# Kernel tuning notes

Measured on AMD Instinct MI355X. Metric: run time of the kernel, lower is better.

Reference implementation:

```python
import jax, jax.numpy as jnp
import numpy as np

N = 50000
E = 800000
D_IN = 128
D_HID = 512
D_OUT = 128
BN_EPS = 1e-5


def setup_inputs() -> dict:
    key = jax.random.key(0)
    ks = jax.random.split(key, 12)
    inp = {}
    inp["v"] = jax.random.normal(ks[0], (N, D_IN), dtype=jnp.float32)
    inp["src"] = jax.random.randint(ks[1], (E,), 0, N, dtype=jnp.int32)
    inp["dst"] = jax.random.randint(ks[2], (E,), 0, N, dtype=jnp.int32)
    inp["edge_weight"] = jax.random.uniform(ks[3], (E,), dtype=jnp.float32)
    # learned parameters
    inp["epsilon"] = jnp.zeros((1, 1), dtype=jnp.float32)  # nn.Parameter([[0.0]])
    s1 = 1.0 / np.sqrt(D_IN)
    s2 = 1.0 / np.sqrt(D_HID)
    inp["W1"] = jax.random.uniform(ks[4], (D_IN, D_HID), minval=-s1, maxval=s1, dtype=jnp.float32)
    inp["b1"] = jax.random.uniform(ks[5], (D_HID,), minval=-s1, maxval=s1, dtype=jnp.float32)
    inp["gamma1"] = jnp.ones((D_HID,), dtype=jnp.float32)
    inp["beta1"] = jnp.zeros((D_HID,), dtype=jnp.float32)
    inp["W2"] = jax.random.uniform(ks[6], (D_HID, D_OUT), minval=-s2, maxval=s2, dtype=jnp.float32)
    inp["b2"] = jax.random.uniform(ks[7], (D_OUT,), minval=-s2, maxval=s2, dtype=jnp.float32)
    inp["gamma2"] = jnp.ones((D_OUT,), dtype=jnp.float32)
    inp["beta2"] = jnp.zeros((D_OUT,), dtype=jnp.float32)
    return inp


def _batchnorm(x, gamma, beta):
    # training-mode BN: batch mean / biased variance over the node axis
    mean = jnp.mean(x, axis=0)
    var = jnp.mean(jnp.square(x - mean), axis=0)
    return gamma * (x - mean) * jax.lax.rsqrt(var + BN_EPS) + beta


def reference(v, src, dst, edge_weight, epsilon, W1, b1, gamma1, beta1, W2, b2, gamma2, beta2):
    n = v.shape[0]
    # sparse.mm(a, v): out[dst] += w * v[src]
    msgs = v[src] * edge_weight[:, None]               # [E, D_IN]
    v_agg = jax.ops.segment_sum(msgs, dst, num_segments=n)  # [N, D_IN]
    v_agg = v_agg + epsilon * v                        # epsilon residual
    h = jax.nn.relu(_batchnorm(v_agg @ W1 + b1, gamma1, beta1))
    out = jax.nn.relu(_batchnorm(h @ W2 + b2, gamma2, beta2))
    return out
```

## Files before the change

### kernel.cpp

```cpp
#include <hip/hip_runtime.h>

#define N_NODES 50000
#define E_EDGES 800000
#define D_INF   128
#define D_HIDF  512
#define D_OUTF  128
#define SCAN_NB ((N_NODES + 255) / 256)
#define M1BLKS  ((N_NODES + 255) / 256)
#define FBLKS   ((N_NODES + 63) / 64)
#define EQ8     (E_EDGES / 8)

#define HIST_NB  ((EQ8 + 255) / 256)
#define CAST_NB  3125
#define PREPW_NB 256
#define PREP_ALL_NB (HIST_NB + CAST_NB + 2 * PREPW_NB)

typedef unsigned short u16;
typedef __attribute__((ext_vector_type(8))) short short8;
typedef __attribute__((ext_vector_type(4))) float floatx4;
typedef const __attribute__((address_space(1))) void gas_t;
typedef __attribute__((address_space(3))) void las_t;

__device__ __forceinline__ u16 f2bf(float f) {
    union { float f; unsigned u; } v; v.f = f;
    unsigned r = (v.u + 0x7fffu + ((v.u >> 16) & 1u)) >> 16;
    return (u16)r;
}
__device__ __forceinline__ float bf2f(u16 b) {
    union { unsigned u; float f; } v; v.u = ((unsigned)b) << 16; return v.f;
}

__global__ __launch_bounds__(256) void prep_all_kernel(
        const float* __restrict__ v, const float* __restrict__ W1,
        const float* __restrict__ W2, const int* __restrict__ dst,
        u16* __restrict__ vbf, u16* __restrict__ W1t, u16* __restrict__ W2t,
        int* __restrict__ counts, int* __restrict__ pos) {
    int b = blockIdx.x;
    int tid = threadIdx.x;
    if (b < HIST_NB) {
        int t = b * 256 + tid;
        if (t >= EQ8) return;
        int d[8], p[8];
#pragma unroll
        for (int k = 0; k < 8; ++k) d[k] = dst[t + k * EQ8];
#pragma unroll
        for (int k = 0; k < 8; ++k) p[k] = atomicAdd(&counts[d[k]], 1);
#pragma unroll
        for (int k = 0; k < 8; ++k) pos[t + k * EQ8] = p[k];
    } else if (b < HIST_NB + CAST_NB) {
        int i = (b - HIST_NB) * 256 + tid;
        const float4 a = ((const float4*)v)[i * 2];
        const float4 c = ((const float4*)v)[i * 2 + 1];
        u16 o[8];
        o[0] = f2bf(a.x); o[1] = f2bf(a.y); o[2] = f2bf(a.z); o[3] = f2bf(a.w);
        o[4] = f2bf(c.x); o[5] = f2bf(c.y); o[6] = f2bf(c.z); o[7] = f2bf(c.w);
        ((float4*)vbf)[i] = *(const float4*)o;
    } else if (b < HIST_NB + CAST_NB + PREPW_NB) {
        int idx = (b - HIST_NB - CAST_NB) * 256 + tid;
        int k1 = idx >> 9, n1 = idx & 511;
        W1t[n1 * 128 + k1] = f2bf(W1[idx]);
    } else {
        int idx = (b - HIST_NB - CAST_NB - PREPW_NB) * 256 + tid;
        int k2 = idx >> 7, n2 = idx & 127;
        W2t[n2 * 512 + k2] = f2bf(W2[idx]);
    }
}

__global__ __launch_bounds__(256) void reduce_kernel(const int* __restrict__ counts,
                                                     int* __restrict__ block_sums) {
    __shared__ int lsum[4];
    int tid = threadIdx.x;
    int gid = blockIdx.x * 256 + tid;
    int s = (gid < N_NODES) ? counts[gid] : 0;
#pragma unroll
    for (int off = 32; off; off >>= 1) s += __shfl_down(s, off);
    if ((tid & 63) == 0) lsum[tid >> 6] = s;
    __syncthreads();
    if (tid == 0) block_sums[blockIdx.x] = lsum[0] + lsum[1] + lsum[2] + lsum[3];
}

__global__ __launch_bounds__(256) void scan_final(const int* __restrict__ counts,
                                                  const int* __restrict__ block_sums,
                                                  int* __restrict__ row_start) {
    __shared__ int sh[256];
    __shared__ int bs[256];
    int tid = threadIdx.x;
    int gid = blockIdx.x * 256 + tid;
    sh[tid] = (gid < N_NODES) ? counts[gid] : 0;
    bs[tid] = (tid < SCAN_NB) ? block_sums[tid] : 0;
    __syncthreads();
    for (int off = 1; off < 256; off <<= 1) {
        int t1 = (tid >= off) ? sh[tid - off] : 0;
        int t2 = (tid >= off) ? bs[tid - off] : 0;
        __syncthreads();
        sh[tid] += t1;
        bs[tid] += t2;
        __syncthreads();
    }
    int boff = (blockIdx.x == 0) ? 0 : bs[blockIdx.x - 1];
    int excl = (tid == 0) ? 0 : sh[tid - 1];
    if (gid < N_NODES) row_start[gid] = boff + excl;
    if (gid == 0) row_start[N_NODES] = E_EDGES;
}

__global__ void fill_kernel(const int* __restrict__ src, const int* __restrict__ dst,
                            const float* __restrict__ w, const int* __restrict__ pos,
                            const int* __restrict__ row_start,
                            int2* __restrict__ csr_ew) {
    int e = blockIdx.x * blockDim.x + threadIdx.x;
    if (e >= E_EDGES) return;
    int d = dst[e];
    int idx = row_start[d] + pos[e];
    int2 rec;
    rec.x = src[e];
    rec.y = __float_as_int(w[e]);
    csr_ew[idx] = rec;
}

__global__ __launch_bounds__(256) void gather_kernel(const u16* __restrict__ vbf,
                                                     const int* __restrict__ row_start,
                                                     const int2* __restrict__ csr_ew,
                                                     const float* __restrict__ eps_p,
                                                     u16* __restrict__ vagg) {
    int node = blockIdx.x * 16 + (threadIdx.x >> 4);
    if (node >= N_NODES) return;
    int c8 = (threadIdx.x & 15) << 3;
    int beg = row_start[node];
    int end = row_start[node + 1];
    float a[8] = {};
    int j = beg;
    for (; j + 1 < end; j += 2) {
        int2 e0 = csr_ew[j];
        int2 e1 = csr_ew[j + 1];
        float w0 = __int_as_float(e0.y);
        float w1 = __int_as_float(e1.y);
        float4 r0 = *(const float4*)(vbf + (size_t)e0.x * D_INF + c8);
        float4 r1 = *(const float4*)(vbf + (size_t)e1.x * D_INF + c8);
        const u16* p0 = (const u16*)&r0;
        const u16* p1 = (const u16*)&r1;
#pragma unroll
        for (int t = 0; t < 8; ++t) a[t] += w0 * bf2f(p0[t]);
#pragma unroll
        for (int t = 0; t < 8; ++t) a[t] += w1 * bf2f(p1[t]);
    }
    if (j < end) {
        int2 e0 = csr_ew[j];
        float w0 = __int_as_float(e0.y);
        float4 r0 = *(const float4*)(vbf + (size_t)e0.x * D_INF + c8);
        const u16* p0 = (const u16*)&r0;
#pragma unroll
        for (int t = 0; t < 8; ++t) a[t] += w0 * bf2f(p0[t]);
    }
    float e = eps_p[0];
    float4 rn = *(const float4*)(vbf + (size_t)node * D_INF + c8);
    const u16* pn = (const u16*)&rn;
    u16 o[8];
#pragma unroll
    for (int t = 0; t < 8; ++t) o[t] = f2bf(a[t] + e * bf2f(pn[t]));
    *(float4*)(vagg + (size_t)node * D_INF + c8) = *(const float4*)o;
}

__global__ __launch_bounds__(512) void stats_gemm1(
        const u16* __restrict__ A, const u16* __restrict__ Bt,
        const float* __restrict__ bias,
        float* __restrict__ psum, float* __restrict__ psq, int M) {
    __shared__ __align__(16) char smem[24576];
    u16* As = (u16*)smem;
    u16* Bs = (u16*)(smem + 16384);
    const int bm = blockIdx.y * 256;
    const int bn = blockIdx.x * 128;
    const int tid = threadIdx.x;
    const int wave = tid >> 6, lane = tid & 63;
    const int wr = wave >> 1, wc = wave & 1;
    const int wm = wr * 64, wn = wc * 64;
    const int lm = lane & 15, quad = lane >> 4;
    floatx4 acc[4][4] = {};
    for (int ks = 0; ks < 4; ++ks) {
        const int k0 = ks << 5;
        {
            const int sub = lane >> 2, s = lane & 3;
#pragma unroll
            for (int t = 0; t < 3; ++t) {
                int ch = wave * 3 + t;
                if (ch < 16) {
                    int row = ch * 16 + sub;
                    int grow = bm + row; if (grow > M - 1) grow = M - 1;
                    int ss = s ^ (row & 3);
                    __builtin_amdgcn_global_load_lds(
                        (gas_t*)(A + (size_t)grow * 128 + k0 + ss * 8),
                        (las_t*)(As + row * 32 + s * 8), 16, 0, 0);
                } else {
                    int row = (ch - 16) * 16 + sub;
                    int ss = s ^ (row & 3);
                    __builtin_amdgcn_global_load_lds(
                        (gas_t*)(Bt + (size_t)(bn + row) * 128 + k0 + ss * 8),
                        (las_t*)(Bs + row * 32 + s * 8), 16, 0, 0);
                }
            }
        }
        __syncthreads();
        short8 af[4], bfr[4];
#pragma unroll
        for (int i = 0; i < 4; ++i) {
            int row = wm + i * 16 + lm;
            af[i] = *(const short8*)&As[row * 32 + ((quad ^ (row & 3)) * 8)];
        }
#pragma unroll
        for (int j = 0; j < 4; ++j) {
            int row = wn + j * 16 + lm;
            bfr[j] = *(const short8*)&Bs[row * 32 + ((quad ^ (row & 3)) * 8)];
        }
#pragma unroll
        for (int i = 0; i < 4; ++i)
#pragma unroll
            for (int j = 0; j < 4; ++j)
                acc[i][j] = __builtin_amdgcn_mfma_f32_16x16x32_bf16(af[i], bfr[j], acc[i][j], 0, 0, 0);
        __syncthreads();
    }
    float* redS = (float*)smem;
    float* redQ = redS + 128;
    if (tid < 128) { redS[tid] = 0.f; redQ[tid] = 0.f; }
    __syncthreads();
#pragma unroll
    for (int j = 0; j < 4; ++j) {
        int cl = wn + j * 16 + lm;
        float bj = bias[bn + cl];
        float s = 0.f, q = 0.f;
#pragma unroll
        for (int i = 0; i < 4; ++i) {
            int row0 = bm + wm + i * 16 + quad * 4;
#pragma unroll
            for (int r = 0; r < 4; ++r)
                if (row0 + r < M) { float x = acc[i][j][r] + bj; s += x; q += x * x; }
        }
        s += __shfl_xor(s, 16); q += __shfl_xor(q, 16);
        s += __shfl_xor(s, 32); q += __shfl_xor(q, 32);
        if (quad == 0) { atomicAdd(&redS[cl], s); atomicAdd(&redQ[cl], q); }
    }
    __syncthreads();
    if (tid < 128) {
        psum[(size_t)blockIdx.y * 512 + bn + tid] = redS[tid];
        psq [(size_t)blockIdx.y * 512 + bn + tid] = redQ[tid];
    }
}

__global__ __launch_bounds__(512, 4) void fused_mlp(
        const u16* __restrict__ vagg, const u16* __restrict__ W1t,
        const u16* __restrict__ W2t,
        const float* __restrict__ b1, const float* __restrict__ scale1,
        const float* __restrict__ shift1, const float* __restrict__ b2,
        u16* __restrict__ x2, float* __restrict__ psum, float* __restrict__ psq,
        int M) {
    __shared__ __align__(16) char smem[49152];
    u16* As  = (u16*)smem;
    u16* W1s = (u16*)(smem + 16384);
    u16* W2s = (u16*)smem;
    u16* hs  = (u16*)(smem + 16384);
    const int bm = blockIdx.x * 64;
    const int tid = threadIdx.x;
    const int wave = tid >> 6, lane = tid & 63;
    const int wr = wave >> 2, wc = wave & 3;
    const int wm = wr * 32;
    const int wn1 = wc * 128;
    const int wn2 = wc * 32;
    const int lm = lane & 15, quad = lane >> 4;

    floatx4 acc1[2][8] = {};
    floatx4 acc2[2][2] = {};

    auto stage_w1 = [&](int win) {
#pragma unroll
        for (int u = 0; u < 4; ++u) {
            int c = tid + u * 512;
            int col = c >> 2, s = c & 3;
            __builtin_amdgcn_global_load_lds(
                (gas_t*)(W1t + (size_t)col * 128 + win * 32 + ((s ^ (col & 3)) * 8)),
                (las_t*)(W1s + col * 32 + s * 8), 16, 0, 0);
        }
    };
    auto stage_w2 = [&](int p, int w) {
#pragma unroll
        for (int u = 0; u < 2; ++u) {
            int c = tid + u * 512;
            int n = c >> 3, s = c & 7;
            __builtin_amdgcn_global_load_lds(
                (gas_t*)(W2t + (size_t)n * 512 + w * 128 + p * 64 + ((s ^ (n & 7)) * 8)),
                (las_t*)(W2s + n * 64 + s * 8), 16, 0, 0);
        }
    };
    auto compute1 = [&](int win) {
        short8 a[2], b[8];
#pragma unroll
        for (int i = 0; i < 2; ++i) {
            int row = wm + i * 16 + lm;
            a[i] = *(const short8*)&As[row * 128 + (((win * 4 + quad) ^ (row & 7)) * 8)];
        }
#pragma unroll
        for (int j = 0; j < 8; ++j) {
            int col = wn1 + j * 16 + lm;
            b[j] = *(const short8*)&W1s[col * 32 + ((quad ^ (col & 3)) * 8)];
        }
#pragma unroll
        for (int i = 0; i < 2; ++i)
#pragma unroll
            for (int j = 0; j < 8; ++j)
                acc1[i][j] = __builtin_amdgcn_mfma_f32_16x16x32_bf16(a[i], b[j], acc1[i][j], 0, 0, 0);
    };
    auto compute2 = [&](int w, int ks) {
        short8 a[2], b[2];
#pragma unroll
        for (int i = 0; i < 2; ++i) {
            int row = wm + i * 16 + lm;
            a[i] = *(const short8*)&hs[row * 256 + (((w * 8 + ks * 4 + quad) ^ (row & 7)) * 8)];
        }
#pragma unroll
        for (int j = 0; j < 2; ++j) {
            int n = wn2 + j * 16 + lm;
            b[j] = *(const short8*)&W2s[n * 64 + (((ks * 4 + quad) ^ (n & 7)) * 8)];
        }
#pragma unroll
        for (int i = 0; i < 2; ++i)
#pragma unroll
            for (int j = 0; j < 2; ++j)
                acc2[i][j] = __builtin_amdgcn_mfma_f32_16x16x32_bf16(a[i], b[j], acc2[i][j], 0, 0, 0);
    };
    auto store_h = [&](int p) {
        float hsc[4], hsh[4];
#pragma unroll
        for (int j = 0; j < 4; ++j) {
            int col = wn1 + (p * 4 + j) * 16 + lm;
            float sc = scale1[col];
            hsc[j] = sc;
            hsh[j] = shift1[col] + sc * b1[col];
        }
#pragma unroll
        for (int i = 0; i < 2; ++i)
#pragma unroll
            for (int j = 0; j < 4; ++j)
#pragma unroll
                for (int r = 0; r < 4; ++r) {
                    int row = wm + i * 16 + quad * 4 + r;
                    int kp = wc * 64 + j * 16 + lm;
                    float hv = fmaxf(0.f, acc1[i][p * 4 + j][r] * hsc[j] + hsh[j]);
                    hs[row * 256 + (((kp >> 3) ^ (row & 7)) * 8) + (kp & 7)] = f2bf(hv);
                }
    };

#pragma unroll
    for (int u = 0; u < 2; ++u) {
        int c = tid + u * 512;
        int row = c >> 4, s = c & 15;
        int grow = bm + row; if (grow > M - 1) grow = M - 1;
        __builtin_amdgcn_global_load_lds(
            (gas_t*)(vagg + (size_t)grow * 128 + ((s ^ (row & 7)) * 8)),
            (las_t*)(As + row * 128 + s * 8), 16, 0, 0);
    }
    stage_w1(0);
    __syncthreads();
    compute1(0);
    __syncthreads();
    stage_w1(1);
    __syncthreads();
    compute1(1);
    __syncthreads();
    stage_w1(2);
    __syncthreads();
    compute1(2);
    __syncthreads();
    stage_w1(3);
    __syncthreads();
    compute1(3);
    __syncthreads();

#pragma unroll
    for (int p = 0; p < 2; ++p) {
        stage_w2(p, 0);
        store_h(p);
        __syncthreads();
#pragma unroll
        for (int w = 0; w < 4; ++w) {
            compute2(w, 0); compute2(w, 1);
            __syncthreads();
            if (w < 3) { stage_w2(p, w + 1); __syncthreads(); }
        }
    }

    float* redS = (float*)smem;
    float* redQ = redS + 128;
    if (tid < 128) { redS[tid] = 0.f; redQ[tid] = 0.f; }
    __syncthreads();
    float bj2[2];
#pragma unroll
    for (int j = 0; j < 2; ++j) {
        int cl = wn2 + j * 16 + lm;
        bj2[j] = b2[cl];
        float s = 0.f, q = 0.f;
#pragma unroll
        for (int i = 0; i < 2; ++i) {
            int row0 = bm + wm + i * 16 + quad * 4;
#pragma unroll
            for (int r = 0; r < 4; ++r)
                if (row0 + r < M) { float x = acc2[i][j][r] + bj2[j]; s += x; q += x * x; }
        }
        s += __shfl_xor(s, 16); q += __shfl_xor(q, 16);
        s += __shfl_xor(s, 32); q += __shfl_xor(q, 32);
        if (quad == 0) { atomicAdd(&redS[cl], s); atomicAdd(&redQ[cl], q); }
    }
    __syncthreads();
    if (tid < 128) {
        psum[(size_t)blockIdx.x * 128 + tid] = redS[tid];
        psq [(size_t)blockIdx.x * 128 + tid] = redQ[tid];
    }
    __syncthreads();

    float* obuf = (float*)smem;
#pragma unroll
    for (int i = 0; i < 2; ++i)
#pragma unroll
        for (int j = 0; j < 2; ++j)
#pragma unroll
            for (int r = 0; r < 4; ++r) {
                int row = wm + i * 16 + quad * 4 + r;
                int col = wn2 + j * 16 + lm;
                obuf[row * 132 + col] = acc2[i][j][r] + bj2[j];
            }
    __syncthreads();
    {
        int row = tid >> 3, seg = (tid & 7) * 16;
        int grow = bm + row;
        if (grow < M) {
            u16 ob[16];
#pragma unroll
            for (int t = 0; t < 4; ++t) {
                float4 f = *(float4*)&obuf[row * 132 + seg + t * 4];
                ob[t * 4 + 0] = f2bf(f.x);
                ob[t * 4 + 1] = f2bf(f.y);
                ob[t * 4 + 2] = f2bf(f.z);
                ob[t * 4 + 3] = f2bf(f.w);
            }
            u16* dp = x2 + (size_t)grow * 128 + seg;
            *(float4*)dp       = *(float4*)ob;
            *(float4*)(dp + 8) = *(float4*)(ob + 8);
        }
    }
}

__global__ __launch_bounds__(1024) void bn_finalize_kernel(
        const float* __restrict__ psum, const float* __restrict__ psq,
        const float* __restrict__ gamma, const float* __restrict__ beta,
        float* __restrict__ scale, float* __restrict__ shift,
        int nblocks, int Ncols, float inv_n) {
    __shared__ float shS[16][64];
    __shared__ float shQ[16][64];
    const int tx = threadIdx.x;
    const int ty = threadIdx.y;
    const int c = blockIdx.x * 64 + tx;
    float s = 0.f, q = 0.f;
    for (int b = ty; b < nblocks; b += 16) {
        s += psum[(size_t)b * Ncols + c];
        q += psq [(size_t)b * Ncols + c];
    }
    shS[ty][tx] = s;
    shQ[ty][tx] = q;
    __syncthreads();
    if (ty == 0) {
        float S = 0.f, Q = 0.f;
#pragma unroll
        for (int r = 0; r < 16; ++r) { S += shS[r][tx]; Q += shQ[r][tx]; }
        float m = S * inv_n;
        float var = Q * inv_n - m * m;
        float rs = rsqrtf(var + 1e-5f);
        float sc = gamma[c] * rs;
        scale[c] = sc;
        shift[c] = beta[c] - sc * m;
    }
}

__global__ void bn2_apply_kernel(const u16* __restrict__ X, float* __restrict__ Y,
                                 const float* __restrict__ scale,
                                 const float* __restrict__ shift, int n8) {
    int i = blockIdx.x * blockDim.x + threadIdx.x;
    if (i >= n8) return;
    int c = (i & 15) << 3;
    float4 raw = ((const float4*)X)[i];
    const u16* xb = (const u16*)&raw;
    float4 sc0 = *(const float4*)(scale + c);
    float4 sc1 = *(const float4*)(scale + c + 4);
    float4 sh0 = *(const float4*)(shift + c);
    float4 sh1 = *(const float4*)(shift + c + 4);
    float4 y0, y1;
    y0.x = fmaxf(0.f, bf2f(xb[0]) * sc0.x + sh0.x);
    y0.y = fmaxf(0.f, bf2f(xb[1]) * sc0.y + sh0.y);
    y0.z = fmaxf(0.f, bf2f(xb[2]) * sc0.z + sh0.z);
    y0.w = fmaxf(0.f, bf2f(xb[3]) * sc0.w + sh0.w);
    y1.x = fmaxf(0.f, bf2f(xb[4]) * sc1.x + sh1.x);
    y1.y = fmaxf(0.f, bf2f(xb[5]) * sc1.y + sh1.y);
    y1.z = fmaxf(0.f, bf2f(xb[6]) * sc1.z + sh1.z);
    y1.w = fmaxf(0.f, bf2f(xb[7]) * sc1.w + sh1.w);
    ((float4*)Y)[i * 2]     = y0;
    ((float4*)Y)[i * 2 + 1] = y1;
}

extern "C" void kernel_launch(void* const* d_in, const int* in_sizes, int n_in,
                              void* d_out, int out_size, void* d_ws, size_t ws_size,
                              hipStream_t stream) {
    const float* v    = (const float*)d_in[0];
    const int* src    = (const int*)d_in[1];
    const int* dst    = (const int*)d_in[2];
    const float* ew   = (const float*)d_in[3];
    const float* eps  = (const float*)d_in[4];
    const float* W1   = (const float*)d_in[5];
    const float* b1   = (const float*)d_in[6];
    const float* g1   = (const float*)d_in[7];
    const float* be1  = (const float*)d_in[8];
    const float* W2   = (const float*)d_in[9];
    const float* b2   = (const float*)d_in[10];
    const float* g2   = (const float*)d_in[11];
    const float* be2  = (const float*)d_in[12];
    float* out = (float*)d_out;

    char* base = (char*)d_ws;
    u16* vbf  = (u16*)(base + 51200000ull);
    u16* vagg = (u16*)(base + 64000000ull);
    u16* x2   = (u16*)(base + 76800000ull);
    u16* W1t  = (u16*)(base + 89600000ull);
    u16* W2t  = (u16*)(base + 89731072ull);
    float* psum   = (float*)(base + 89862144ull);
    float* psq    = (float*)(base + 90663168ull);
    float* scale1 = (float*)(base + 91464192ull);
    float* shift1 = scale1 + 512;
    float* scale2 = shift1 + 512;
    float* shift2 = scale2 + 128;
    int* counts     = (int*)(shift2 + 128);
    int* row_start  = counts + 50000;
    int* pos        = row_start + 50004;
    int2* csr_ew    = (int2*)(pos + 800000);
    int* block_sums = (int*)(csr_ew + 800000);

    hipMemsetAsync(counts, 0, (size_t)50000 * sizeof(int), stream);

    prep_all_kernel<<<PREP_ALL_NB, 256, 0, stream>>>(v, W1, W2, dst, vbf, W1t, W2t,
                                                     counts, pos);
    reduce_kernel<<<SCAN_NB, 256, 0, stream>>>(counts, block_sums);
    scan_final<<<SCAN_NB, 256, 0, stream>>>(counts, block_sums, row_start);
    fill_kernel<<<(E_EDGES + 255) / 256, 256, 0, stream>>>(src, dst, ew, pos, row_start, csr_ew);
    gather_kernel<<<(N_NODES + 15) / 16, 256, 0, stream>>>(vbf, row_start, csr_ew, eps, vagg);

    {
        dim3 grid(D_HIDF / 128, M1BLKS);
        stats_gemm1<<<grid, 512, 0, stream>>>(vagg, W1t, b1, psum, psq, N_NODES);
    }
    bn_finalize_kernel<<<D_HIDF / 64, dim3(64, 16), 0, stream>>>(
        psum, psq, g1, be1, scale1, shift1, M1BLKS, D_HIDF, 1.0f / N_NODES);

    fused_mlp<<<FBLKS, 512, 0, stream>>>(vagg, W1t, W2t, b1, scale1, shift1, b2,
                                         x2, psum, psq, N_NODES);
    bn_finalize_kernel<<<D_OUTF / 64, dim3(64, 16), 0, stream>>>(
        psum, psq, g2, be2, scale2, shift2, FBLKS, D_OUTF, 1.0f / N_NODES);

    {
        int n8 = N_NODES * D_OUTF / 8;
        bn2_apply_kernel<<<(n8 + 255) / 256, 256, 0, stream>>>(x2, out, scale2, shift2, n8);
    }
}
```

Baseline: 270.3 us.

## Fuse BN finalize into GEMM kernels via last-block reduction; shrink pos to u16

```diff
diff --git a/kernel.cpp b/kernel.cpp
--- a/kernel.cpp
+++ b/kernel.cpp
@@ -7,6 +7,7 @@
 #define D_OUTF  128
 #define SCAN_NB ((N_NODES + 255) / 256)
 #define M1BLKS  ((N_NODES + 255) / 256)
+#define S1BLKS  (4 * M1BLKS)
 #define FBLKS   ((N_NODES + 63) / 64)
 #define EQ8     (E_EDGES / 8)
 
@@ -34,7 +35,7 @@
         const float* __restrict__ v, const float* __restrict__ W1,
         const float* __restrict__ W2, const int* __restrict__ dst,
         u16* __restrict__ vbf, u16* __restrict__ W1t, u16* __restrict__ W2t,
-        int* __restrict__ counts, int* __restrict__ pos) {
+        int* __restrict__ counts, u16* __restrict__ pos) {
     int b = blockIdx.x;
     int tid = threadIdx.x;
     if (b < HIST_NB) {
@@ -46,7 +47,7 @@
 #pragma unroll
         for (int k = 0; k < 8; ++k) p[k] = atomicAdd(&counts[d[k]], 1);
 #pragma unroll
-        for (int k = 0; k < 8; ++k) pos[t + k * EQ8] = p[k];
+        for (int k = 0; k < 8; ++k) pos[t + k * EQ8] = (u16)p[k];
     } else if (b < HIST_NB + CAST_NB) {
         int i = (b - HIST_NB) * 256 + tid;
         const float4 a = ((const float4*)v)[i * 2];
@@ -104,13 +105,13 @@
 }
 
 __global__ void fill_kernel(const int* __restrict__ src, const int* __restrict__ dst,
-                            const float* __restrict__ w, const int* __restrict__ pos,
+                            const float* __restrict__ w, const u16* __restrict__ pos,
                             const int* __restrict__ row_start,
                             int2* __restrict__ csr_ew) {
     int e = blockIdx.x * blockDim.x + threadIdx.x;
     if (e >= E_EDGES) return;
     int d = dst[e];
-    int idx = row_start[d] + pos[e];
+    int idx = row_start[d] + (int)pos[e];
     int2 rec;
     rec.x = src[e];
     rec.y = __float_as_int(w[e]);
@@ -163,8 +164,12 @@
 __global__ __launch_bounds__(512) void stats_gemm1(
         const u16* __restrict__ A, const u16* __restrict__ Bt,
         const float* __restrict__ bias,
-        float* __restrict__ psum, float* __restrict__ psq, int M) {
+        float* __restrict__ psum, float* __restrict__ psq,
+        const float* __restrict__ g1, const float* __restrict__ be1,
+        float* __restrict__ scale1, float* __restrict__ shift1,
+        int* __restrict__ done1, int M) {
     __shared__ __align__(16) char smem[24576];
+    __shared__ int lastf;
     u16* As = (u16*)smem;
     u16* Bs = (u16*)(smem + 16384);
     const int bm = blockIdx.y * 256;
@@ -242,6 +247,25 @@
         psum[(size_t)blockIdx.y * 512 + bn + tid] = redS[tid];
         psq [(size_t)blockIdx.y * 512 + bn + tid] = redQ[tid];
     }
+
+    __threadfence();
+    if (tid == 0) lastf = (atomicAdd(done1, 1) == S1BLKS - 1) ? 1 : 0;
+    __syncthreads();
+    if (lastf) {
+        __threadfence();
+        float s = 0.f, q = 0.f;
+        for (int b = 0; b < M1BLKS; ++b) {
+            s += psum[(size_t)b * 512 + tid];
+            q += psq [(size_t)b * 512 + tid];
+        }
+        const float inv_n = 1.0f / (float)N_NODES;
+        float m = s * inv_n;
+        float var = q * inv_n - m * m;
+        float rs = rsqrtf(var + 1e-5f);
+        float sc = g1[tid] * rs;
+        scale1[tid] = sc;
+        shift1[tid] = be1[tid] - sc * m;
+    }
 }
 
 __global__ __launch_bounds__(512, 4) void fused_mlp(
@@ -250,8 +274,11 @@
         const float* __restrict__ b1, const float* __restrict__ scale1,
         const float* __restrict__ shift1, const float* __restrict__ b2,
         u16* __restrict__ x2, float* __restrict__ psum, float* __restrict__ psq,
-        int M) {
+        const float* __restrict__ g2, const float* __restrict__ be2,
+        float* __restrict__ scale2, float* __restrict__ shift2,
+        int* __restrict__ done2, int M) {
     __shared__ __align__(16) char smem[49152];
+    __shared__ int lastf;
     u16* As  = (u16*)smem;
     u16* W1s = (u16*)(smem + 16384);
     u16* W2s = (u16*)smem;
@@ -443,36 +470,33 @@
             *(float4*)(dp + 8) = *(float4*)(ob + 8);
         }
     }
-}
-
-__global__ __launch_bounds__(1024) void bn_finalize_kernel(
-        const float* __restrict__ psum, const float* __restrict__ psq,
-        const float* __restrict__ gamma, const float* __restrict__ beta,
-        float* __restrict__ scale, float* __restrict__ shift,
-        int nblocks, int Ncols, float inv_n) {
-    __shared__ float shS[16][64];
-    __shared__ float shQ[16][64];
-    const int tx = threadIdx.x;
-    const int ty = threadIdx.y;
-    const int c = blockIdx.x * 64 + tx;
-    float s = 0.f, q = 0.f;
-    for (int b = ty; b < nblocks; b += 16) {
-        s += psum[(size_t)b * Ncols + c];
-        q += psq [(size_t)b * Ncols + c];
-    }
-    shS[ty][tx] = s;
-    shQ[ty][tx] = q;
-    __syncthreads();
-    if (ty == 0) {
-        float S = 0.f, Q = 0.f;
-#pragma unroll
-        for (int r = 0; r < 16; ++r) { S += shS[r][tx]; Q += shQ[r][tx]; }
-        float m = S * inv_n;
-        float var = Q * inv_n - m * m;
-        float rs = rsqrtf(var + 1e-5f);
-        float sc = gamma[c] * rs;
-        scale[c] = sc;
-        shift[c] = beta[c] - sc * m;
+
+    __threadfence();
+    if (tid == 0) lastf = (atomicAdd(done2, 1) == FBLKS - 1) ? 1 : 0;
+    __syncthreads();
+    if (lastf) {
+        __threadfence();
+        float* fr = (float*)smem;
+        int c = tid & 127, part = tid >> 7;
+        float s = 0.f, q = 0.f;
+        for (int b = part; b < FBLKS; b += 4) {
+            s += psum[(size_t)b * 128 + c];
+            q += psq [(size_t)b * 128 + c];
+        }
+        fr[part * 128 + c] = s;
+        fr[512 + part * 128 + c] = q;
+        __syncthreads();
+        if (tid < 128) {
+            float S = fr[tid] + fr[128 + tid] + fr[256 + tid] + fr[384 + tid];
+            float Q = fr[512 + tid] + fr[640 + tid] + fr[768 + tid] + fr[896 + tid];
+            const float inv_n = 1.0f / (float)N_NODES;
+            float m = S * inv_n;
+            float var = Q * inv_n - m * m;
+            float rs = rsqrtf(var + 1e-5f);
+            float sc = g2[tid] * rs;
+            scale2[tid] = sc;
+            shift2[tid] = be2[tid] - sc * m;
+        }
     }
 }
 
@@ -532,12 +556,14 @@
     float* scale2 = shift1 + 512;
     float* shift2 = scale2 + 128;
     int* counts     = (int*)(shift2 + 128);
-    int* row_start  = counts + 50000;
-    int* pos        = row_start + 50004;
-    int2* csr_ew    = (int2*)(pos + 800000);
+    int* done1      = counts + 50000;
+    int* done2      = counts + 50001;
+    int* row_start  = counts + 50008;
+    u16* pos        = (u16*)(row_start + 50004);
+    int2* csr_ew    = (int2*)((char*)pos + 1600000ull);
     int* block_sums = (int*)(csr_ew + 800000);
 
-    hipMemsetAsync(counts, 0, (size_t)50000 * sizeof(int), stream);
+    hipMemsetAsync(counts, 0, (size_t)50008 * sizeof(int), stream);
 
     prep_all_kernel<<<PREP_ALL_NB, 256, 0, stream>>>(v, W1, W2, dst, vbf, W1t, W2t,
                                                      counts, pos);
@@ -548,15 +574,13 @@
 
     {
         dim3 grid(D_HIDF / 128, M1BLKS);
-        stats_gemm1<<<grid, 512, 0, stream>>>(vagg, W1t, b1, psum, psq, N_NODES);
-    }
-    bn_finalize_kernel<<<D_HIDF / 64, dim3(64, 16), 0, stream>>>(
-        psum, psq, g1, be1, scale1, shift1, M1BLKS, D_HIDF, 1.0f / N_NODES);
+        stats_gemm1<<<grid, 512, 0, stream>>>(vagg, W1t, b1, psum, psq,
+                                              g1, be1, scale1, shift1, done1, N_NODES);
+    }
 
     fused_mlp<<<FBLKS, 512, 0, stream>>>(vagg, W1t, W2t, b1, scale1, shift1, b2,
-                                         x2, psum, psq, N_NODES);
-    bn_finalize_kernel<<<D_OUTF / 64, dim3(64, 16), 0, stream>>>(
-        psum, psq, g2, be2, scale2, shift2, FBLKS, D_OUTF, 1.0f / N_NODES);
+                                         x2, psum, psq, g2, be2, scale2, shift2,
+                                         done2, N_NODES);
 
     {
         int n8 = N_NODES * D_OUTF / 8;
```

Result: slower. 606.0 us (+124.2%).
